# Optimization experiments

Hardware: AMD Instinct MI355X
Metric: run time of the kernel (lower is better)

## Reference

```python
import jax, jax.numpy as jnp
import numpy as np

F, N, H = 1024, 16, 64  # features, num_heads, head_dim
B, T, S = 2, 1024, 2048  # batch, query len, memory (kv) len
M = S + 1                # relative position embeddings length


def _relative_shift(x):
    # x: [B, N, T, M] -> [B, N, T, M-1]  (Transformer-XL relative shift)
    b, h, q_len, k_len = x.shape
    x = jnp.pad(x, ((0, 0), (0, 0), (0, 0), (1, 0)))
    x = x.reshape(b, h, k_len + 1, q_len)
    x = x[:, :, 1:, :]
    x = x.reshape(b, h, q_len, k_len)
    return x[..., :-1]


def setup_inputs() -> dict:
    key = jax.random.key(0)
    ks = jax.random.split(key, 12)
    s = 1.0 / np.sqrt(F)
    return {
        'x': jax.random.normal(ks[0], (B, T, F), jnp.float32),
        'rel': jax.random.normal(ks[1], (M, F), jnp.float32),
        'memory': jax.random.normal(ks[2], (B, S, F), jnp.float32),
        'Wq': jax.random.normal(ks[3], (F, N, H), jnp.float32) * s,
        'Wk': jax.random.normal(ks[4], (F, N, H), jnp.float32) * s,
        'Wv': jax.random.normal(ks[5], (F, N, H), jnp.float32) * s,
        'Wr': jax.random.normal(ks[6], (F, N, H), jnp.float32) * s,
        'u_bias': jnp.zeros((N, H), jnp.float32),
        'v_bias': jnp.zeros((N, H), jnp.float32),
        'Wout': jax.random.normal(ks[7], (N * H, F), jnp.float32) * (1.0 / np.sqrt(N * H)),
        'b_out': jnp.zeros((F,), jnp.float32),
    }


def reference(x, rel, memory, Wq, Wk, Wv, Wr, u_bias, v_bias, Wout, b_out):
    b, t = x.shape[0], x.shape[1]
    # projections (DenseGeneral, no bias)
    q = jnp.einsum('btf,fnh->btnh', x, Wq)
    k = jnp.einsum('bsf,fnh->bsnh', memory, Wk)
    v = jnp.einsum('bsf,fnh->bsnh', memory, Wv)
    r = jnp.einsum('mf,fnh->mnh', rel, Wr)
    head_dim = q.shape[-1]
    scale = 1.0 / jnp.sqrt(jnp.asarray(head_dim, jnp.float32))
    q_u = q + u_bias[None, None]
    q_v = q + v_bias[None, None]
    # relative position bias, materialized at [B,N,T,M] then shifted
    bd = jnp.einsum('btnh,mnh->bntm', q_v, r)
    bd = _relative_shift(bd)                        # [B,N,T,S]
    bias = (bd * scale).astype(jnp.float32)
    # attention (dot_product_attention math), q/k/v in bf16 per source
    qb = q_u.astype(jnp.bfloat16)
    kb = k.astype(jnp.bfloat16)
    vb = v.astype(jnp.bfloat16)
    logits = jnp.einsum('btnh,bsnh->bnts', qb, kb).astype(jnp.float32) * scale + bias
    probs = jax.nn.softmax(logits, axis=-1)         # fp32 softmax
    out = jnp.einsum('bnts,bsnh->btnh', probs.astype(jnp.bfloat16), vb)
    out = out.astype(jnp.float32).reshape(b, t, -1)  # [B,T,N*H]
    return out @ Wout + b_out
```

## Files before the change

### kernel.cpp

```cpp
#include <hip/hip_runtime.h>
#include <cmath>

#define C_SCALE 0.18033688011112042f

typedef __attribute__((ext_vector_type(8))) short bf16x8;
typedef __attribute__((ext_vector_type(8))) _Float16 half8;
typedef __attribute__((ext_vector_type(4))) _Float16 half4;
typedef __attribute__((ext_vector_type(4))) float f32x4;
typedef __attribute__((ext_vector_type(4))) unsigned short us4;

__device__ inline unsigned short bf16_rne(float f) {
    unsigned u = __builtin_bit_cast(unsigned, f);
    u += 0x7fff + ((u >> 16) & 1);
    return (unsigned short)(u >> 16);
}

__device__ inline void lds_dma16(const _Float16* g, _Float16* l) {
    __builtin_amdgcn_global_load_lds(
        (__attribute__((address_space(1))) void*)(void*)g,
        (__attribute__((address_space(3))) void*)(void*)l, 16, 0, 0);
}

__global__ __launch_bounds__(256) void prep_kernel(
    const float* __restrict__ x, const float* __restrict__ mem,
    const float* __restrict__ rel,
    const float* __restrict__ s0, const float* __restrict__ s1,
    const float* __restrict__ s2, const float* __restrict__ s3,
    const float* __restrict__ s4,
    _Float16* __restrict__ x16, _Float16* __restrict__ mem16,
    _Float16* __restrict__ rel16,
    _Float16* __restrict__ d0, _Float16* __restrict__ d1,
    _Float16* __restrict__ d2, _Float16* __restrict__ d3,
    _Float16* __restrict__ d4)
{
    const int bx = blockIdx.x, tid = threadIdx.x;
    if (bx < 1280) {
        __shared__ _Float16 T[64][72];
        const int z = bx >> 8, rem = bx & 255;
        const float* src = z == 0 ? s0 : z == 1 ? s1 : z == 2 ? s2 : z == 3 ? s3 : s4;
        _Float16*    dst = z == 0 ? d0 : z == 1 ? d1 : z == 2 ? d2 : z == 3 ? d3 : d4;
        const int r0 = (rem & 15) * 64, c0 = (rem >> 4) * 64;
        const int r = tid >> 4, c4 = (tid & 15) * 4;
        #pragma unroll
        for (int rr = 0; rr < 64; rr += 16) {
            float4 v = *(const float4*)(src + (size_t)(r0 + r + rr) * 1024 + c0 + c4);
            T[c4 + 0][r + rr] = (_Float16)v.x;
            T[c4 + 1][r + rr] = (_Float16)v.y;
            T[c4 + 2][r + rr] = (_Float16)v.z;
            T[c4 + 3][r + rr] = (_Float16)v.w;
        }
        __syncthreads();
        const int orow = tid >> 2, seg = (tid & 3) * 16;
        half8 h0 = *(const half8*)&T[orow][seg];
        half8 h1 = *(const half8*)&T[orow][seg + 8];
        *(half8*)(dst + (size_t)(c0 + orow) * 1024 + r0 + seg)     = h0;
        *(half8*)(dst + (size_t)(c0 + orow) * 1024 + r0 + seg + 8) = h1;
    } else {
        size_t i = ((size_t)(bx - 1280) * 256 + tid) * 8;
        if (i >= 8389632ull) return;
        const float* src; _Float16* dst; size_t off;
        if (i < 2097152ull)      { src = x;   dst = x16;   off = i; }
        else if (i < 6291456ull) { src = mem; dst = mem16; off = i - 2097152ull; }
        else                     { src = rel; dst = rel16; off = i - 6291456ull; }
        float4 a = *(const float4*)(src + off);
        float4 b = *(const float4*)(src + off + 4);
        half8 h;
        h[0]=(_Float16)a.x; h[1]=(_Float16)a.y; h[2]=(_Float16)a.z; h[3]=(_Float16)a.w;
        h[4]=(_Float16)b.x; h[5]=(_Float16)b.y; h[6]=(_Float16)b.z; h[7]=(_Float16)b.w;
        *(half8*)(dst + off) = h;
    }
}

__global__ __launch_bounds__(256) void proj3_kernel(
    const _Float16* __restrict__ x16, const _Float16* __restrict__ mem16,
    const _Float16* __restrict__ rel16,
    const _Float16* __restrict__ Wqt, const _Float16* __restrict__ Wkt,
    const _Float16* __restrict__ Wvt, const _Float16* __restrict__ Wrt,
    const float* __restrict__ ub, const float* __restrict__ vb,
    unsigned short* __restrict__ qu, _Float16* __restrict__ qv,
    unsigned short* __restrict__ kb, unsigned short* __restrict__ vtb,
    _Float16* __restrict__ rb)
{
    alignas(16) __shared__ _Float16 As[128 * 64];
    alignas(16) __shared__ _Float16 Bs[128 * 64];
    const int tid = threadIdx.x;
    const int lane = tid & 63, w = tid >> 6, c = lane & 15, g = lane >> 4;
    const int bx = blockIdx.x, col0 = blockIdx.y * 128;

    int mode, row0, rowmax;
    const _Float16 *Ap, *Bp;
    if (bx < 16)      { mode = 0; row0 = bx * 128;        rowmax = 2047; Ap = x16;   Bp = Wqt; }
    else if (bx < 48) { mode = 1; row0 = (bx - 16) * 128; rowmax = 4095; Ap = mem16; Bp = Wkt; }
    else if (bx < 80) { mode = 2; row0 = (bx - 48) * 128; rowmax = 4095; Ap = mem16; Bp = Wvt; }
    else              { mode = 3; row0 = (bx - 80) * 128; rowmax = 2048; Ap = rel16; Bp = Wrt; }

    const int qr = (w & 1) * 64, qc = (w >> 1) * 64;
    const int srow = lane >> 3, phys = lane & 7;
    f32x4 acc[4][4] = {};

    for (int k0 = 0; k0 < 1024; k0 += 64) {
        #pragma unroll
        for (int q = 0; q < 4; q++) {
            int row = 32 * w + 8 * q + srow;
            int log = phys ^ (row & 7);
            int ar = row0 + row; if (ar > rowmax) ar = rowmax;
            lds_dma16(Ap + (size_t)ar * 1024 + k0 + log * 8, &As[(32 * w + 8 * q) * 64]);
            lds_dma16(Bp + (size_t)(col0 + row) * 1024 + k0 + log * 8, &Bs[(32 * w + 8 * q) * 64]);
        }
        __syncthreads();
        #pragma unroll
        for (int s = 0; s < 2; s++) {
            half8 af[4], bf[4];
            #pragma unroll
            for (int i = 0; i < 4; i++) {
                int row = qr + 16 * i + c;
                af[i] = *(const half8*)&As[row * 64 + ((4 * s + g) ^ (row & 7)) * 8];
            }
            #pragma unroll
            for (int j = 0; j < 4; j++) {
                int row = qc + 16 * j + c;
                bf[j] = *(const half8*)&Bs[row * 64 + ((4 * s + g) ^ (row & 7)) * 8];
            }
            #pragma unroll
            for (int i = 0; i < 4; i++)
                #pragma unroll
                for (int j = 0; j < 4; j++)
                    acc[i][j] = __builtin_amdgcn_mfma_f32_16x16x32_f16(af[i], bf[j], acc[i][j], 0, 0, 0);
        }
        __syncthreads();
    }

    #pragma unroll
    for (int i = 0; i < 4; i++) {
        #pragma unroll
        for (int j = 0; j < 4; j++) {
            const int cg = col0 + qc + 16 * j + c;
            const int rbase = row0 + qr + 16 * i + 4 * g;
            if (mode == 0) {
                float u = ub[cg], v = vb[cg];
                #pragma unroll
                for (int rg = 0; rg < 4; rg++) {
                    size_t o = (size_t)(rbase + rg) * 1024 + cg;
                    qu[o] = bf16_rne(acc[i][j][rg] + u);
                    qv[o] = (_Float16)((acc[i][j][rg] + v) * C_SCALE);
                }
            } else if (mode == 1) {
                #pragma unroll
                for (int rg = 0; rg < 4; rg++)
                    kb[(size_t)(rbase + rg) * 1024 + cg] = bf16_rne(acc[i][j][rg]);
            } else if (mode == 2) {
                us4 pk;
                #pragma unroll
                for (int rg = 0; rg < 4; rg++) pk[rg] = bf16_rne(acc[i][j][rg]);
                int b = rbase >> 11, s = rbase & 2047;
                *(us4*)&vtb[((size_t)(b * 16 + (cg >> 6)) * 64 + (cg & 63)) * 2048 + s] = pk;
            } else {
                #pragma unroll
                for (int rg = 0; rg < 4; rg++) {
                    int r_g = rbase + rg;
                    if (r_g < 2049)
                        rb[((size_t)(cg >> 6) * 2049 + r_g) * 64 + (cg & 63)] = (_Float16)acc[i][j][rg];
                }
            }
        }
    }
}

__global__ __launch_bounds__(256) void flash_kernel(
    const unsigned short* __restrict__ qu, const _Float16* __restrict__ qv,
    const unsigned short* __restrict__ kg, const unsigned short* __restrict__ vt,
    const _Float16* __restrict__ rb, _Float16* __restrict__ po, float* __restrict__ pl)
{
    __shared__ unsigned short Ks[64][70];
    __shared__ unsigned short Vs[64][70];
    __shared__ unsigned short Ps[64][70];
    __shared__ _Float16 BDT[128][70];
    const int tid = threadIdx.x;
    const int lane = tid & 63, w = tid >> 6, c = lane & 15, g = lane >> 4;
    const int id = blockIdx.x;
    const int p_pair = id & 127;
    const int t0 = (id >> 7) * 64;
    const int bn = p_pair >> 2, part = p_pair & 3;
    const int b = bn >> 4, n = bn & 15;
    const int s_start = part * 512;

    const unsigned short* qp = qu + (size_t)(b * 1024 + t0 + 16 * w + c) * 1024 + n * 64 + g * 8;
    bf16x8 qf0 = *(const bf16x8*)qp;
    bf16x8 qf1 = *(const bf16x8*)(qp + 32);
    const _Float16* qvp = qv + (size_t)(b * 1024 + t0 + 16 * w + c) * 1024 + n * 64 + g * 8;
    half8 av0 = *(const half8*)qvp;
    half8 av1 = *(const half8*)(qvp + 32);
    int r2 = t0 + 16 * w + c + 1; if (r2 > 1023) r2 = 1023;
    const _Float16* qvp2 = qv + (size_t)(b * 1024 + r2) * 1024 + n * 64 + g * 8;
    half8 aw0 = *(const half8*)qvp2;
    half8 aw1 = *(const half8*)(qvp2 + 32);

    const _Float16* rbase = rb + (size_t)n * 2049 * 64;

    f32x4 o[4] = {};
    float l_i[4] = {0.f, 0.f, 0.f, 0.f};

    const int sr = tid >> 2, scc = (tid & 3) * 16;
    const unsigned short* kstage = kg + (size_t)(b * 2048 + s_start + sr) * 1024 + n * 64 + scc;
    const unsigned short* vstage = vt + ((size_t)bn * 64 + sr) * 2048 + s_start + scc;

    auto r_ptr = [&](int Dl) {
        int mm = (Dl <= 1026) ? (Dl + 1023 > 2048 ? 2048 : Dl + 1023) : Dl - 1027;
        return rbase + (size_t)mm * 64 + g * 8;
    };
    auto bd_one = [&](int Dbase, int j, half8 r0, half8 r1) {
        int Dl = Dbase + 16 * j + c;
        int Dmin = Dbase + 16 * j;
        f32x4 z;
        if (Dmin + 15 <= 1026) {
            f32x4 zm = {};
            zm = __builtin_amdgcn_mfma_f32_16x16x32_f16(av0, r0, zm, 0, 0, 0);
            zm = __builtin_amdgcn_mfma_f32_16x16x32_f16(av1, r1, zm, 0, 0, 0);
            z = zm;
        } else if (Dmin >= 1027) {
            f32x4 zw = {};
            zw = __builtin_amdgcn_mfma_f32_16x16x32_f16(aw0, r0, zw, 0, 0, 0);
            zw = __builtin_amdgcn_mfma_f32_16x16x32_f16(aw1, r1, zw, 0, 0, 0);
            z = zw;
        } else {
            f32x4 zm = {}, zw = {};
            zm = __builtin_amdgcn_mfma_f32_16x16x32_f16(av0, r0, zm, 0, 0, 0);
            zm = __builtin_amdgcn_mfma_f32_16x16x32_f16(av1, r1, zm, 0, 0, 0);
            zw = __builtin_amdgcn_mfma_f32_16x16x32_f16(aw0, r0, zw, 0, 0, 0);
            zw = __builtin_amdgcn_mfma_f32_16x16x32_f16(aw1, r1, zw, 0, 0, 0);
            z = (Dl >= 1027) ? zw : zm;
        }
        if (Dl == 1026) { z[0] = 0.f; z[1] = 0.f; z[2] = 0.f; z[3] = 0.f; }
        half4 hv;
        #pragma unroll
        for (int rg = 0; rg < 4; rg++) hv[rg] = (_Float16)z[rg];
        *(half4*)&BDT[Dl & 127][16 * w + 4 * g] = hv;
    };

    const int d0 = s_start - t0;
    half8 rx[8], rr[8];
    #pragma unroll
    for (int j = 0; j < 4; j++) {
        const _Float16* rp = r_ptr(d0 - 63 + 16 * j + c);
        rx[2 * j] = *(const half8*)rp; rx[2 * j + 1] = *(const half8*)(rp + 32);
    }
    #pragma unroll
    for (int j = 0; j < 4; j++) {
        const _Float16* rp = r_ptr(d0 + 1 + 16 * j + c);
        rr[2 * j] = *(const half8*)rp; rr[2 * j + 1] = *(const half8*)(rp + 32);
    }
    uint4 k0r = *(const uint4*)(kstage);
    uint4 k1r = *(const uint4*)(kstage + 8);
    uint4 v0r = *(const uint4*)(vstage);
    uint4 v1r = *(const uint4*)(vstage + 8);

    for (int kk = 0; kk < 8; kk++) {
        const int diff0 = d0 + kk * 64;

        *(uint4*)&Ks[sr][scc]     = k0r;
        *(uint4*)&Ks[sr][scc + 8] = k1r;
        *(uint4*)&Vs[sr][scc]     = v0r;
        *(uint4*)&Vs[sr][scc + 8] = v1r;
        if (kk == 0) {
            #pragma unroll
            for (int j = 0; j < 4; j++) bd_one(d0 - 63, j, rx[2 * j], rx[2 * j + 1]);
        }
        #pragma unroll
        for (int j = 0; j < 4; j++) bd_one(diff0 + 1, j, rr[2 * j], rr[2 * j + 1]);

        __syncthreads();

        const int kn = kk < 7 ? kk + 1 : 7;
        k0r = *(const uint4*)(kstage + (size_t)(kn * 64) * 1024);
        k1r = *(const uint4*)(kstage + (size_t)(kn * 64) * 1024 + 8);
        v0r = *(const uint4*)(vstage + kn * 64);
        v1r = *(const uint4*)(vstage + kn * 64 + 8);
        const int Dn = diff0 + 65;
        #pragma unroll
        for (int j = 0; j < 4; j++) {
            const _Float16* rp = r_ptr(Dn + 16 * j + c);
            rr[2 * j] = *(const half8*)rp; rr[2 * j + 1] = *(const half8*)(rp + 32);
        }

        #pragma unroll
        for (int j = 0; j < 4; j++) {
            bf16x8 kf0 = *(const bf16x8*)&Ks[16 * j + c][g * 8];
            bf16x8 kf1 = *(const bf16x8*)&Ks[16 * j + c][32 + g * 8];
            f32x4 sa = {};
            sa = __builtin_amdgcn_mfma_f32_16x16x32_bf16(qf0, kf0, sa, 0, 0, 0);
            sa = __builtin_amdgcn_mfma_f32_16x16x32_bf16(qf1, kf1, sa, 0, 0, 0);
            #pragma unroll
            for (int rg = 0; rg < 4; rg++) {
                int tt = 16 * w + 4 * g + rg;
                int D = diff0 + 16 * j + c - tt;
                float bdt = (float)BDT[D & 127][tt];
                float p = exp2f(fmaf(sa[rg], C_SCALE, bdt));
                l_i[rg] += p;
                Ps[tt][16 * j + c] = bf16_rne(p);
            }
        }

        bf16x8 pf0 = *(const bf16x8*)&Ps[16 * w + c][g * 8];
        bf16x8 pf1 = *(const bf16x8*)&Ps[16 * w + c][32 + g * 8];
        #pragma unroll
        for (int j = 0; j < 4; j++) {
            bf16x8 vf0 = *(const bf16x8*)&Vs[16 * j + c][g * 8];
            bf16x8 vf1 = *(const bf16x8*)&Vs[16 * j + c][32 + g * 8];
            o[j] = __builtin_amdgcn_mfma_f32_16x16x32_bf16(pf0, vf0, o[j], 0, 0, 0);
            o[j] = __builtin_amdgcn_mfma_f32_16x16x32_bf16(pf1, vf1, o[j], 0, 0, 0);
        }
        __syncthreads();
    }

    #pragma unroll
    for (int rg = 0; rg < 4; rg++) {
        float s2 = l_i[rg];
        #pragma unroll
        for (int off = 1; off < 16; off <<= 1)
            s2 += __shfl_xor(s2, off, 16);
        int t = t0 + 16 * w + 4 * g + rg;
        size_t rowb = ((size_t)part * 32 + bn) * 1024 + t;
        if (c == 0) pl[rowb] = s2;
        float inv = 1.f / s2;
        #pragma unroll
        for (int j = 0; j < 4; j++)
            po[rowb * 64 + 16 * j + c] = (_Float16)(o[j][rg] * inv);
    }
}

__global__ __launch_bounds__(256) void combine_kernel(
    const _Float16* __restrict__ po, const float* __restrict__ pl,
    _Float16* __restrict__ attn)
{
    int f = blockIdx.x * 256 + threadIdx.x;
    int h = f & 63, t = (f >> 6) & 1023, bn = f >> 16;
    float os = 0.f, ls = 0.f;
    #pragma unroll
    for (int p = 0; p < 4; p++) {
        size_t rowb = ((size_t)p * 32 + bn) * 1024 + t;
        float lp = pl[rowb];
        os += lp * (float)po[rowb * 64 + h];
        ls += lp;
    }
    int b = bn >> 4, n = bn & 15;
    attn[((size_t)b * 1024 + t) * 1024 + n * 64 + h] = (_Float16)(os / ls);
}

__global__ __launch_bounds__(256) void out2_kernel(
    const _Float16* __restrict__ A, const _Float16* __restrict__ Bt,
    const float* __restrict__ bias, float* __restrict__ out)
{
    alignas(16) __shared__ _Float16 As[4096];
    alignas(16) __shared__ _Float16 Bs[4096];
    const int tid = threadIdx.x;
    const int lane = tid & 63, w = tid >> 6, c = lane & 15, g = lane >> 4;
    const int row0 = blockIdx.x * 64, col0 = blockIdx.y * 64;
    const int srow = 16 * w + (lane >> 3);
    const int phys = lane & 7;
    f32x4 acc[4] = {};

    for (int k0 = 0; k0 < 1024; k0 += 64) {
        #pragma unroll
        for (int q = 0; q < 2; q++) {
            int row = srow + 8 * q;
            int log = phys ^ (row & 7);
            lds_dma16(A  + (size_t)(row0 + row) * 1024 + k0 + log * 8, &As[(16 * w + 8 * q) * 64]);
            lds_dma16(Bt + (size_t)(col0 + row) * 1024 + k0 + log * 8, &Bs[(16 * w + 8 * q) * 64]);
        }
        __syncthreads();
        #pragma unroll
        for (int s = 0; s < 2; s++) {
            const int pc = ((4 * s + g) ^ (c & 7)) * 8;
            half8 af = *(const half8*)&As[(16 * w + c) * 64 + pc];
            #pragma unroll
            for (int j = 0; j < 4; j++) {
                half8 bf = *(const half8*)&Bs[(16 * j + c) * 64 + pc];
                acc[j] = __builtin_amdgcn_mfma_f32_16x16x32_f16(af, bf, acc[j], 0, 0, 0);
            }
        }
        __syncthreads();
    }
    #pragma unroll
    for (int j = 0; j < 4; j++)
        #pragma unroll
        for (int rg = 0; rg < 4; rg++) {
            int r_g = row0 + 16 * w + g * 4 + rg, cg = col0 + 16 * j + c;
            out[(size_t)r_g * 1024 + cg] = acc[j][rg] + bias[cg];
        }
}

extern "C" void kernel_launch(void* const* d_in, const int* in_sizes, int n_in,
                              void* d_out, int out_size, void* d_ws, size_t ws_size,
                              hipStream_t stream)
{
    const float* x    = (const float*)d_in[0];
    const float* rel  = (const float*)d_in[1];
    const float* mem  = (const float*)d_in[2];
    const float* Wq   = (const float*)d_in[3];
    const float* Wk   = (const float*)d_in[4];
    const float* Wv   = (const float*)d_in[5];
    const float* Wr   = (const float*)d_in[6];
    const float* ub   = (const float*)d_in[7];
    const float* vb   = (const float*)d_in[8];
    const float* Wout = (const float*)d_in[9];
    const float* bout = (const float*)d_in[10];
    float* out = (float*)d_out;

    char* ws = (char*)d_ws;
    unsigned short* qu    = (unsigned short*)(ws);
    _Float16*       qv    = (_Float16*)(ws + (4ull << 20));
    unsigned short* kb    = (unsigned short*)(ws + (8ull << 20));
    unsigned short* vtb   = (unsigned short*)(ws + (16ull << 20));
    _Float16*       rb    = (_Float16*)(ws + (24ull << 20));
    _Float16*       attn  = (_Float16*)(ws + (29ull << 20));
    _Float16*       po    = (_Float16*)(ws + (33ull << 20));
    float*          pl    = (float*)(ws + (50ull << 20));
    _Float16*       x16   = (_Float16*)(ws + (51ull << 20));
    _Float16*       mem16 = (_Float16*)(ws + (55ull << 20));
    _Float16*       rel16 = (_Float16*)(ws + (63ull << 20));
    _Float16*       Wqt   = (_Float16*)(ws + (68ull << 20));
    _Float16*       Wkt   = (_Float16*)(ws + (70ull << 20));
    _Float16*       Wvt   = (_Float16*)(ws + (72ull << 20));
    _Float16*       Wrt   = (_Float16*)(ws + (74ull << 20));
    _Float16*       Woutt = (_Float16*)(ws + (76ull << 20));

    prep_kernel<<<dim3(5377), 256, 0, stream>>>(
        x, mem, rel, Wq, Wk, Wv, Wr, Wout,
        x16, mem16, rel16, Wqt, Wkt, Wvt, Wrt, Woutt);
    proj3_kernel<<<dim3(97, 8), 256, 0, stream>>>(
        x16, mem16, rel16, Wqt, Wkt, Wvt, Wrt, ub, vb, qu, qv, kb, vtb, rb);
    flash_kernel<<<dim3(2048), 256, 0, stream>>>(qu, qv, kb, vtb, rb, po, pl);
    combine_kernel<<<dim3(8192), 256, 0, stream>>>(po, pl, attn);
    out2_kernel<<<dim3(32, 16), 256, 0, stream>>>(attn, Woutt, bout, out);
}
```

Baseline: 280.3 us.

## Read K/V directly from global in flash kernel and enlarge output GEMM tiles

The flash kernel no longer stages K and V tiles through shared memory. Each wave loads its MFMA fragments straight from global memory, which removes the K/V LDS arrays and the per-iteration __syncthreads barriers, and it sets launch_bounds to 4 blocks per CU. The relative-position bias tile for the next step is now computed after the softmax phase instead of before a barrier, and its r loads are issued inline rather than prefetched. The output projection moves from 64x64 to 128x128 tiles with a 4x4 MFMA accumulator per wave, giving more reuse per LDS load. The trade-off is redundant global and L2 traffic, since every wave reloads the same K/V, plus higher register pressure in the larger GEMM. Dropping the barriers between Ps writes and reads across iterations may also be a race hazard, although each wave appears to touch only its own rows.

```diff
diff --git a/kernel.cpp b/kernel.cpp
--- a/kernel.cpp
+++ b/kernel.cpp
@@ -166,15 +166,13 @@
     }
 }
 
-__global__ __launch_bounds__(256) void flash_kernel(
+__global__ __launch_bounds__(256, 4) void flash_kernel(
     const unsigned short* __restrict__ qu, const _Float16* __restrict__ qv,
     const unsigned short* __restrict__ kg, const unsigned short* __restrict__ vt,
     const _Float16* __restrict__ rb, _Float16* __restrict__ po, float* __restrict__ pl)
 {
-    __shared__ unsigned short Ks[64][70];
-    __shared__ unsigned short Vs[64][70];
-    __shared__ unsigned short Ps[64][70];
-    __shared__ _Float16 BDT[128][70];
+    __shared__ unsigned short Ps[64 * 70];
+    __shared__ _Float16 BDT[128 * 70];
     const int tid = threadIdx.x;
     const int lane = tid & 63, w = tid >> 6, c = lane & 15, g = lane >> 4;
     const int id = blockIdx.x;
@@ -196,21 +194,19 @@
     half8 aw1 = *(const half8*)(qvp2 + 32);
 
     const _Float16* rbase = rb + (size_t)n * 2049 * 64;
+    const unsigned short* kR = kg + (size_t)(b * 2048 + s_start + c) * 1024 + n * 64 + g * 8;
+    const unsigned short* vR = vt + ((size_t)bn * 64 + c) * 2048 + s_start + g * 8;
 
     f32x4 o[4] = {};
     float l_i[4] = {0.f, 0.f, 0.f, 0.f};
 
-    const int sr = tid >> 2, scc = (tid & 3) * 16;
-    const unsigned short* kstage = kg + (size_t)(b * 2048 + s_start + sr) * 1024 + n * 64 + scc;
-    const unsigned short* vstage = vt + ((size_t)bn * 64 + sr) * 2048 + s_start + scc;
-
-    auto r_ptr = [&](int Dl) {
-        int mm = (Dl <= 1026) ? (Dl + 1023 > 2048 ? 2048 : Dl + 1023) : Dl - 1027;
-        return rbase + (size_t)mm * 64 + g * 8;
-    };
-    auto bd_one = [&](int Dbase, int j, half8 r0, half8 r1) {
+    auto bd_one = [&](int Dbase, int j) {
         int Dl = Dbase + 16 * j + c;
         int Dmin = Dbase + 16 * j;
+        int mm = (Dl <= 1026) ? (Dl + 1023 > 2048 ? 2048 : Dl + 1023) : Dl - 1027;
+        const _Float16* rp = rbase + (size_t)mm * 64 + g * 8;
+        half8 r0 = *(const half8*)rp;
+        half8 r1 = *(const half8*)(rp + 32);
         f32x4 z;
         if (Dmin + 15 <= 1026) {
             f32x4 zm = {};
@@ -234,58 +230,21 @@
         half4 hv;
         #pragma unroll
         for (int rg = 0; rg < 4; rg++) hv[rg] = (_Float16)z[rg];
-        *(half4*)&BDT[Dl & 127][16 * w + 4 * g] = hv;
+        *(half4*)&BDT[(Dl & 127) * 70 + 16 * w + 4 * g] = hv;
     };
 
     const int d0 = s_start - t0;
-    half8 rx[8], rr[8];
     #pragma unroll
-    for (int j = 0; j < 4; j++) {
-        const _Float16* rp = r_ptr(d0 - 63 + 16 * j + c);
-        rx[2 * j] = *(const half8*)rp; rx[2 * j + 1] = *(const half8*)(rp + 32);
-    }
-    #pragma unroll
-    for (int j = 0; j < 4; j++) {
-        const _Float16* rp = r_ptr(d0 + 1 + 16 * j + c);
-        rr[2 * j] = *(const half8*)rp; rr[2 * j + 1] = *(const half8*)(rp + 32);
-    }
-    uint4 k0r = *(const uint4*)(kstage);
-    uint4 k1r = *(const uint4*)(kstage + 8);
-    uint4 v0r = *(const uint4*)(vstage);
-    uint4 v1r = *(const uint4*)(vstage + 8);
+    for (int j = 0; j < 8; j++) bd_one(d0 - 63, j);
 
     for (int kk = 0; kk < 8; kk++) {
         const int diff0 = d0 + kk * 64;
 
-        *(uint4*)&Ks[sr][scc]     = k0r;
-        *(uint4*)&Ks[sr][scc + 8] = k1r;
-        *(uint4*)&Vs[sr][scc]     = v0r;
-        *(uint4*)&Vs[sr][scc + 8] = v1r;
-        if (kk == 0) {
-            #pragma unroll
-            for (int j = 0; j < 4; j++) bd_one(d0 - 63, j, rx[2 * j], rx[2 * j + 1]);
-        }
-        #pragma unroll
-        for (int j = 0; j < 4; j++) bd_one(diff0 + 1, j, rr[2 * j], rr[2 * j + 1]);
-
-        __syncthreads();
-
-        const int kn = kk < 7 ? kk + 1 : 7;
-        k0r = *(const uint4*)(kstage + (size_t)(kn * 64) * 1024);
-        k1r = *(const uint4*)(kstage + (size_t)(kn * 64) * 1024 + 8);
-        v0r = *(const uint4*)(vstage + kn * 64);
-        v1r = *(const uint4*)(vstage + kn * 64 + 8);
-        const int Dn = diff0 + 65;
         #pragma unroll
         for (int j = 0; j < 4; j++) {
-            const _Float16* rp = r_ptr(Dn + 16 * j + c);
-            rr[2 * j] = *(const half8*)rp; rr[2 * j + 1] = *(const half8*)(rp + 32);
-        }
-
-        #pragma unroll
-        for (int j = 0; j < 4; j++) {
-            bf16x8 kf0 = *(const bf16x8*)&Ks[16 * j + c][g * 8];
-            bf16x8 kf1 = *(const bf16x8*)&Ks[16 * j + c][32 + g * 8];
+            const unsigned short* kp = kR + (size_t)(kk * 64 + 16 * j) * 1024;
+            bf16x8 kf0 = *(const bf16x8*)kp;
+            bf16x8 kf1 = *(const bf16x8*)(kp + 32);
             f32x4 sa = {};
             sa = __builtin_amdgcn_mfma_f32_16x16x32_bf16(qf0, kf0, sa, 0, 0, 0);
             sa = __builtin_amdgcn_mfma_f32_16x16x32_bf16(qf1, kf1, sa, 0, 0, 0);
@@ -293,23 +252,28 @@
             for (int rg = 0; rg < 4; rg++) {
                 int tt = 16 * w + 4 * g + rg;
                 int D = diff0 + 16 * j + c - tt;
-                float bdt = (float)BDT[D & 127][tt];
+                float bdt = (float)BDT[(D & 127) * 70 + tt];
                 float p = exp2f(fmaf(sa[rg], C_SCALE, bdt));
                 l_i[rg] += p;
-                Ps[tt][16 * j + c] = bf16_rne(p);
-            }
-        }
-
-        bf16x8 pf0 = *(const bf16x8*)&Ps[16 * w + c][g * 8];
-        bf16x8 pf1 = *(const bf16x8*)&Ps[16 * w + c][32 + g * 8];
+                Ps[tt * 70 + 16 * j + c] = bf16_rne(p);
+            }
+        }
+
+        if (kk < 7) {
+            #pragma unroll
+            for (int j = 0; j < 4; j++) bd_one(diff0 + 65, j);
+        }
+
+        bf16x8 pf0 = *(const bf16x8*)&Ps[(16 * w + c) * 70 + g * 8];
+        bf16x8 pf1 = *(const bf16x8*)&Ps[(16 * w + c) * 70 + 32 + g * 8];
         #pragma unroll
         for (int j = 0; j < 4; j++) {
-            bf16x8 vf0 = *(const bf16x8*)&Vs[16 * j + c][g * 8];
-            bf16x8 vf1 = *(const bf16x8*)&Vs[16 * j + c][32 + g * 8];
+            const unsigned short* vp = vR + (size_t)(16 * j) * 2048 + kk * 64;
+            bf16x8 vf0 = *(const bf16x8*)vp;
+            bf16x8 vf1 = *(const bf16x8*)(vp + 32);
             o[j] = __builtin_amdgcn_mfma_f32_16x16x32_bf16(pf0, vf0, o[j], 0, 0, 0);
             o[j] = __builtin_amdgcn_mfma_f32_16x16x32_bf16(pf1, vf1, o[j], 0, 0, 0);
         }
-        __syncthreads();
     }
 
     #pragma unroll
@@ -346,46 +310,58 @@
     attn[((size_t)b * 1024 + t) * 1024 + n * 64 + h] = (_Float16)(os / ls);
 }
 
-__global__ __launch_bounds__(256) void out2_kernel(
+__global__ __launch_bounds__(256) void out3_kernel(
     const _Float16* __restrict__ A, const _Float16* __restrict__ Bt,
     const float* __restrict__ bias, float* __restrict__ out)
 {
-    alignas(16) __shared__ _Float16 As[4096];
-    alignas(16) __shared__ _Float16 Bs[4096];
+    alignas(16) __shared__ _Float16 As[128 * 64];
+    alignas(16) __shared__ _Float16 Bs[128 * 64];
     const int tid = threadIdx.x;
     const int lane = tid & 63, w = tid >> 6, c = lane & 15, g = lane >> 4;
-    const int row0 = blockIdx.x * 64, col0 = blockIdx.y * 64;
-    const int srow = 16 * w + (lane >> 3);
-    const int phys = lane & 7;
-    f32x4 acc[4] = {};
+    const int row0 = blockIdx.x * 128, col0 = blockIdx.y * 128;
+    const int qr = (w & 1) * 64, qc = (w >> 1) * 64;
+    const int srow = lane >> 3, phys = lane & 7;
+    f32x4 acc[4][4] = {};
 
     for (int k0 = 0; k0 < 1024; k0 += 64) {
         #pragma unroll
-        for (int q = 0; q < 2; q++) {
-            int row = srow + 8 * q;
+        for (int q = 0; q < 4; q++) {
+            int row = 32 * w + 8 * q + srow;
             int log = phys ^ (row & 7);
-            lds_dma16(A  + (size_t)(row0 + row) * 1024 + k0 + log * 8, &As[(16 * w + 8 * q) * 64]);
-            lds_dma16(Bt + (size_t)(col0 + row) * 1024 + k0 + log * 8, &Bs[(16 * w + 8 * q) * 64]);
+            lds_dma16(A  + (size_t)(row0 + row) * 1024 + k0 + log * 8, &As[(32 * w + 8 * q) * 64]);
+            lds_dma16(Bt + (size_t)(col0 + row) * 1024 + k0 + log * 8, &Bs[(32 * w + 8 * q) * 64]);
         }
         __syncthreads();
         #pragma unroll
         for (int s = 0; s < 2; s++) {
-            const int pc = ((4 * s + g) ^ (c & 7)) * 8;
-            half8 af = *(const half8*)&As[(16 * w + c) * 64 + pc];
+            half8 af[4], bf[4];
+            #pragma unroll
+            for (int i = 0; i < 4; i++) {
+                int row = qr + 16 * i + c;
+                af[i] = *(const half8*)&As[row * 64 + ((4 * s + g) ^ (row & 7)) * 8];
+            }
             #pragma unroll
             for (int j = 0; j < 4; j++) {
-                half8 bf = *(const half8*)&Bs[(16 * j + c) * 64 + pc];
-                acc[j] = __builtin_amdgcn_mfma_f32_16x16x32_f16(af, bf, acc[j], 0, 0, 0);
-            }
+                int row = qc + 16 * j + c;
+                bf[j] = *(const half8*)&Bs[row * 64 + ((4 * s + g) ^ (row & 7)) * 8];
+            }
+            #pragma unroll
+            for (int i = 0; i < 4; i++)
+                #pragma unroll
+                for (int j = 0; j < 4; j++)
+                    acc[i][j] = __builtin_amdgcn_mfma_f32_16x16x32_f16(af[i], bf[j], acc[i][j], 0, 0, 0);
         }
         __syncthreads();
     }
     #pragma unroll
-    for (int j = 0; j < 4; j++)
-        #pragma unroll
-        for (int rg = 0; rg < 4; rg++) {
-            int r_g = row0 + 16 * w + g * 4 + rg, cg = col0 + 16 * j + c;
-            out[(size_t)r_g * 1024 + cg] = acc[j][rg] + bias[cg];
+    for (int i = 0; i < 4; i++)
+        #pragma unroll
+        for (int j = 0; j < 4; j++) {
+            const int cg = col0 + qc + 16 * j + c;
+            const int rbase = row0 + qr + 16 * i + 4 * g;
+            #pragma unroll
+            for (int rg = 0; rg < 4; rg++)
+                out[(size_t)(rbase + rg) * 1024 + cg] = acc[i][j][rg] + bias[cg];
         }
 }
 
@@ -431,5 +407,5 @@
         x16, mem16, rel16, Wqt, Wkt, Wvt, Wrt, ub, vb, qu, qv, kb, vtb, rb);
     flash_kernel<<<dim3(2048), 256, 0, stream>>>(qu, qv, kb, vtb, rb, po, pl);
     combine_kernel<<<dim3(8192), 256, 0, stream>>>(po, pl, attn);
-    out2_kernel<<<dim3(32, 16), 256, 0, stream>>>(attn, Woutt, bout, out);
-}
+    out3_kernel<<<dim3(16, 8), 256, 0, stream>>>(attn, Woutt, bout, out);
+}
```

New measurement: 365.7 us. 30.5% more time.
